# Kernel tuning notes

Measured on AMD Instinct MI355X. Metric: run time of the kernel, lower is better.

The kernel has to match this reference:

```python
import jax, jax.numpy as jnp
import numpy as np
from jax import lax

H = 128      # hidden width everywhere
L = 4        # GRU layers
N = 32768    # number of atom events / decode steps
V = 3072     # 512 * 6 atom vocab


def _lin(x, w, b):
    return x @ w.T + b


def _lrelu(x):
    return jnp.where(x >= 0, x, 0.2 * x)


def _res(x, w1, b1, w2, b2):
    h = _lrelu(_lin(x, w1, b1))
    return _lrelu(x + _lin(h, w2, b2))


def _res_stack(x, ws1, bs1, ws2, bs2):
    for i in range(ws1.shape[0]):
        x = _res(x, ws1[i], bs1[i], ws2[i], bs2[i])
    return x


def _head(x, ws1, bs1, ws2, bs2, w, b):
    return _lin(_res_stack(x, ws1, bs1, ws2, bs2), w, b)


def _forward(atom, time, mag, atom_emb, mag_w, mag_b, pos_w, pos_b,
             reduce_w, reduce_b, net_w1, net_b1, net_w2, net_b2,
             final_w, final_b, redg_w, redg_b, wg_w1, wg_b1, wg_w2, wg_b2,
             gfinal_w, gfinal_b, gru_wih, gru_whh, gru_bih, gru_bhh,
             ah_w1, ah_b1, ah_w2, ah_b2, ah_w, ah_b,
             ph_w1, ph_b1, ph_w2, ph_b2, ph_w, ph_b,
             mh_w1, mh_b1, mh_w2, mh_b2, mh_w, mh_b):
    n_steps = atom.shape[0]
    # ----- Encoder -----
    ae = atom_emb[atom]                               # [N, 128]
    te = _lin(time[:, None], pos_w, pos_b)            # [N, 128]
    me = _lin(mag[:, None], mag_w, mag_b)             # [N, 128]
    x = _lin(jnp.concatenate([ae, te, me], axis=-1), reduce_w, reduce_b)
    x = _res_stack(x, net_w1, net_b1, net_w2, net_b2)
    x = _lin(x, final_w, final_b)
    g = jnp.sum(x, axis=0, keepdims=True)             # [1, 128]
    x = jnp.concatenate([x, jnp.broadcast_to(g, x.shape)], axis=-1)
    x = _lin(x, redg_w, redg_b)
    x = _res_stack(x, wg_w1, wg_b1, wg_w2, wg_b2)
    x = _lin(x, gfinal_w, gfinal_b)
    z = jnp.sum(x, axis=0, keepdims=True)             # [1, 128]

    # ----- Decoder: 4-layer GRU, output fed back as next input -----
    def gru_step(carry, _):
        inp, hid = carry                              # [128], [L, 128]
        xs = inp
        new_h = []
        for l in range(L):
            gi = gru_wih[l] @ xs + gru_bih[l]         # [384]
            gh = gru_whh[l] @ hid[l] + gru_bhh[l]     # [384]
            ir, iz, inn = jnp.split(gi, 3)
            hr, hz, hn = jnp.split(gh, 3)
            r = jax.nn.sigmoid(ir + hr)
            zt = jax.nn.sigmoid(iz + hz)
            n = jnp.tanh(inn + r * hn)
            hl = (1.0 - zt) * n + zt * hid[l]
            new_h.append(hl)
            xs = hl
        return (xs, jnp.stack(new_h)), xs

    init = (z[0], jnp.zeros((L, H), dtype=z.dtype))
    _, encodings = lax.scan(gru_step, init, None, length=n_steps)  # [N, 128]

    atoms = _head(encodings, ah_w1, ah_b1, ah_w2, ah_b2, ah_w, ah_b)
    pos = jnp.clip(_head(encodings, ph_w1, ph_b1, ph_w2, ph_b2, ph_w, ph_b), 0.0, 1.0)
    mags = _head(encodings, mh_w1, mh_b1, mh_w2, mh_b2, mh_w, mh_b)
    return atoms, pos, mags, z


def setup_inputs():
    key = jax.random.key(0)
    ks = jax.random.split(key, 64)
    it = iter(range(64))

    def nrm(shape, scale=0.05):
        return jax.random.normal(ks[next(it)], shape, dtype=jnp.float32) * scale

    inp = {
        "atom": jax.random.randint(ks[next(it)], (N,), 0, V),
        "time": jax.random.uniform(ks[next(it)], (N,), dtype=jnp.float32),
        "mag": jax.random.uniform(ks[next(it)], (N,), dtype=jnp.float32),
        "atom_emb": nrm((V, H)),
        "mag_w": nrm((H, 1)), "mag_b": nrm((H,)),
        "pos_w": nrm((H, 1)), "pos_b": nrm((H,)),
        "reduce_w": nrm((H, 3 * H)), "reduce_b": nrm((H,)),
        "net_w1": nrm((4, H, H)), "net_b1": nrm((4, H)),
        "net_w2": nrm((4, H, H)), "net_b2": nrm((4, H)),
        "final_w": nrm((H, H)), "final_b": nrm((H,)),
        "redg_w": nrm((H, 2 * H)), "redg_b": nrm((H,)),
        "wg_w1": nrm((4, H, H)), "wg_b1": nrm((4, H)),
        "wg_w2": nrm((4, H, H)), "wg_b2": nrm((4, H)),
        "gfinal_w": nrm((H, H)), "gfinal_b": nrm((H,)),
        "gru_wih": nrm((L, 3 * H, H)), "gru_whh": nrm((L, 3 * H, H)),
        "gru_bih": nrm((L, 3 * H)), "gru_bhh": nrm((L, 3 * H)),
        "ah_w1": nrm((2, H, H)), "ah_b1": nrm((2, H)),
        "ah_w2": nrm((2, H, H)), "ah_b2": nrm((2, H)),
        "ah_w": nrm((H, H)), "ah_b": nrm((H,)),
        "ph_w1": nrm((2, H, H)), "ph_b1": nrm((2, H)),
        "ph_w2": nrm((2, H, H)), "ph_b2": nrm((2, H)),
        "ph_w": nrm((1, H)), "ph_b": nrm((1,)),
        "mh_w1": nrm((2, H, H)), "mh_b1": nrm((2, H)),
        "mh_w2": nrm((2, H, H)), "mh_b2": nrm((2, H)),
        "mh_w": nrm((1, H)), "mh_b": nrm((1,)),
    }
    return inp


def reference(atom, time, mag, atom_emb, mag_w, mag_b, pos_w, pos_b,
              reduce_w, reduce_b, net_w1, net_b1, net_w2, net_b2,
              final_w, final_b, redg_w, redg_b, wg_w1, wg_b1, wg_w2, wg_b2,
              gfinal_w, gfinal_b, gru_wih, gru_whh, gru_bih, gru_bhh,
              ah_w1, ah_b1, ah_w2, ah_b2, ah_w, ah_b,
              ph_w1, ph_b1, ph_w2, ph_b2, ph_w, ph_b,
              mh_w1, mh_b1, mh_w2, mh_b2, mh_w, mh_b):
    return _forward(atom, time, mag, atom_emb, mag_w, mag_b, pos_w, pos_b,
                    reduce_w, reduce_b, net_w1, net_b1, net_w2, net_b2,
                    final_w, final_b, redg_w, redg_b, wg_w1, wg_b1, wg_w2, wg_b2,
                    gfinal_w, gfinal_b, gru_wih, gru_whh, gru_bih, gru_bhh,
                    ah_w1, ah_b1, ah_w2, ah_b2, ah_w, ah_b,
                    ph_w1, ph_b1, ph_w2, ph_b2, ph_w, ph_b,
                    mh_w1, mh_b1, mh_w2, mh_b2, mh_w, mh_b)
```

## Files before the change

kernel.cpp:

```cpp
#include <hip/hip_runtime.h>
#include <hip/hip_bf16.h>

#define NEVT 32768
#define NBLK (NEVT / 8)

typedef _Float16 f16;
typedef _Float16 f16x2 __attribute__((ext_vector_type(2)));
typedef float f32x16 __attribute__((ext_vector_type(16)));
typedef float Row128[128];

#ifndef __has_builtin
#define __has_builtin(x) 0
#endif

__device__ __forceinline__ float dot2f(f16x2 a, f16x2 b, float c) {
#if __has_builtin(__builtin_amdgcn_fdot2)
  return __builtin_amdgcn_fdot2(a, b, c, false);
#else
  return c + (float)a[0] * (float)b[0] + (float)a[1] * (float)b[1];
#endif
}

__device__ __forceinline__ float lrelu(float v) { return v >= 0.f ? v : 0.2f * v; }

__device__ __forceinline__ float sigmoidf(float x) {
  return 1.f / (1.f + __expf(-x));
}

__device__ __forceinline__ float tanh_f(float x) {
  float ax = fabsf(x);
  float e = __expf(-2.f * ax);
  float t = (1.f - e) / (1.f + e);
  return x >= 0.f ? t : -t;
}

__device__ __forceinline__ void res_block(Row128* xb, Row128* hb,
    const float* __restrict__ w1, const float* __restrict__ b1,
    const float* __restrict__ w2, const float* __restrict__ b2, int u) {
  float acc[8];
  float bb = b1[u];
  #pragma unroll
  for (int r = 0; r < 8; ++r) acc[r] = bb;
  #pragma unroll 4
  for (int k = 0; k < 128; ++k) {
    float w = w1[u * 128 + k];
    #pragma unroll
    for (int r = 0; r < 8; ++r) acc[r] += w * xb[r][k];
  }
  #pragma unroll
  for (int r = 0; r < 8; ++r) hb[r][u] = lrelu(acc[r]);
  __syncthreads();
  bb = b2[u];
  #pragma unroll
  for (int r = 0; r < 8; ++r) acc[r] = bb;
  #pragma unroll 4
  for (int k = 0; k < 128; ++k) {
    float w = w2[u * 128 + k];
    #pragma unroll
    for (int r = 0; r < 8; ++r) acc[r] += w * hb[r][k];
  }
  #pragma unroll
  for (int r = 0; r < 8; ++r) xb[r][u] = lrelu(xb[r][u] + acc[r]);
  __syncthreads();
}

__global__ __launch_bounds__(128) void enc1_kernel(
    const int* __restrict__ atom, const float* __restrict__ tvec,
    const float* __restrict__ mvec, const float* __restrict__ atom_emb,
    const float* __restrict__ mag_w, const float* __restrict__ mag_b,
    const float* __restrict__ pos_w, const float* __restrict__ pos_b,
    const float* __restrict__ reduce_w, const float* __restrict__ reduce_b,
    const float* __restrict__ net_w1, const float* __restrict__ net_b1,
    const float* __restrict__ net_w2, const float* __restrict__ net_b2,
    const float* __restrict__ final_w, const float* __restrict__ final_b,
    float* __restrict__ xf, float* __restrict__ pg) {
  const int u = threadIdx.x;
  const int r0 = blockIdx.x * 8;
  __shared__ float xin[8][384];
  __shared__ float xb[8][128];
  __shared__ float hb[8][128];
  #pragma unroll
  for (int r = 0; r < 8; ++r) {
    int row = r0 + r;
    xin[r][u] = atom_emb[atom[row] * 128 + u];
    xin[r][128 + u] = tvec[row] * pos_w[u] + pos_b[u];
    xin[r][256 + u] = mvec[row] * mag_w[u] + mag_b[u];
  }
  __syncthreads();
  float acc[8];
  float bb = reduce_b[u];
  #pragma unroll
  for (int r = 0; r < 8; ++r) acc[r] = bb;
  #pragma unroll 4
  for (int k = 0; k < 384; ++k) {
    float w = reduce_w[u * 384 + k];
    #pragma unroll
    for (int r = 0; r < 8; ++r) acc[r] += w * xin[r][k];
  }
  #pragma unroll
  for (int r = 0; r < 8; ++r) xb[r][u] = acc[r];
  __syncthreads();
  for (int blk = 0; blk < 4; ++blk)
    res_block(xb, hb, net_w1 + blk * 16384, net_b1 + blk * 128,
              net_w2 + blk * 16384, net_b2 + blk * 128, u);
  bb = final_b[u];
  #pragma unroll
  for (int r = 0; r < 8; ++r) acc[r] = bb;
  #pragma unroll 4
  for (int k = 0; k < 128; ++k) {
    float w = final_w[u * 128 + k];
    #pragma unroll
    for (int r = 0; r < 8; ++r) acc[r] += w * xb[r][k];
  }
  float s = 0.f;
  #pragma unroll
  for (int r = 0; r < 8; ++r) {
    xf[(r0 + r) * 128 + u] = acc[r];
    s += acc[r];
  }
  pg[blockIdx.x * 128 + u] = s;
}

__global__ __launch_bounds__(1024) void reduce_kernel(
    const float* __restrict__ src, int m, float* __restrict__ dst) {
  int u = threadIdx.x & 127, c = threadIdx.x >> 7;
  float s = 0.f;
  for (int i = c; i < m; i += 8) s += src[i * 128 + u];
  __shared__ float tmp[8][128];
  tmp[c][u] = s;
  __syncthreads();
  if (c == 0) {
    float t = 0.f;
    #pragma unroll
    for (int j = 0; j < 8; ++j) t += tmp[j][u];
    dst[u] = t;
  }
}

__global__ __launch_bounds__(128) void enc2_kernel(
    const float* __restrict__ xf, const float* __restrict__ g,
    const float* __restrict__ redg_w, const float* __restrict__ redg_b,
    const float* __restrict__ wg_w1, const float* __restrict__ wg_b1,
    const float* __restrict__ wg_w2, const float* __restrict__ wg_b2,
    const float* __restrict__ gfinal_w, const float* __restrict__ gfinal_b,
    float* __restrict__ pz) {
  const int u = threadIdx.x;
  const int r0 = blockIdx.x * 8;
  __shared__ float xin[8][256];
  __shared__ float xb[8][128];
  __shared__ float hb[8][128];
  #pragma unroll
  for (int r = 0; r < 8; ++r) {
    xin[r][u] = xf[(r0 + r) * 128 + u];
    xin[r][128 + u] = g[u];
  }
  __syncthreads();
  float acc[8];
  float bb = redg_b[u];
  #pragma unroll
  for (int r = 0; r < 8; ++r) acc[r] = bb;
  #pragma unroll 4
  for (int k = 0; k < 256; ++k) {
    float w = redg_w[u * 256 + k];
    #pragma unroll
    for (int r = 0; r < 8; ++r) acc[r] += w * xin[r][k];
  }
  #pragma unroll
  for (int r = 0; r < 8; ++r) xb[r][u] = acc[r];
  __syncthreads();
  for (int blk = 0; blk < 4; ++blk)
    res_block(xb, hb, wg_w1 + blk * 16384, wg_b1 + blk * 128,
              wg_w2 + blk * 16384, wg_b2 + blk * 128, u);
  bb = gfinal_b[u];
  #pragma unroll
  for (int r = 0; r < 8; ++r) acc[r] = bb;
  #pragma unroll 4
  for (int k = 0; k < 128; ++k) {
    float w = gfinal_w[u * 128 + k];
    #pragma unroll
    for (int r = 0; r < 8; ++r) acc[r] += w * xb[r][k];
  }
  float s = 0.f;
  #pragma unroll
  for (int r = 0; r < 8; ++r) s += acc[r];
  pz[blockIdx.x * 128 + u] = s;
}

__global__ __launch_bounds__(256) void wprep_kernel(
    const float* __restrict__ wih, const float* __restrict__ whh,
    f16* __restrict__ w16i, f16* __restrict__ w16h) {
  int idx = blockIdx.x * 256 + threadIdx.x;
  if (idx < 196608) {
    w16i[idx] = (f16)wih[idx];
    w16h[idx] = (f16)whh[idx];
  }
}


#define PW(WV, K) __builtin_bit_cast(f16x2, (WV)[(K)])

#define D4(WV, B, Q, A) \
  A = dot2f(PW(WV,(B)+0), __builtin_bit_cast(f16x2,(Q).x), A); \
  A = dot2f(PW(WV,(B)+1), __builtin_bit_cast(f16x2,(Q).y), A); \
  A = dot2f(PW(WV,(B)+2), __builtin_bit_cast(f16x2,(Q).z), A); \
  A = dot2f(PW(WV,(B)+3), __builtin_bit_cast(f16x2,(Q).w), A);

#define D4Q(WQ, Q, A) \
  A = dot2f(__builtin_bit_cast(f16x2,(WQ).x), __builtin_bit_cast(f16x2,(Q).x), A); \
  A = dot2f(__builtin_bit_cast(f16x2,(WQ).y), __builtin_bit_cast(f16x2,(Q).y), A); \
  A = dot2f(__builtin_bit_cast(f16x2,(WQ).z), __builtin_bit_cast(f16x2,(Q).z), A); \
  A = dot2f(__builtin_bit_cast(f16x2,(WQ).w), __builtin_bit_cast(f16x2,(Q).w), A);

#define F32T(WV, K, XS, OFF) { f16x2 p_ = PW(WV, (K)); \
  a0_ += (float)p_[0] * (XS)[(OFF) + 2*(K)]; \
  a1_ += (float)p_[1] * (XS)[(OFF) + 2*(K) + 1]; }

#define F32T16(WV, XS, OFF) \
  F32T(WV,0,XS,OFF) F32T(WV,1,XS,OFF) F32T(WV,2,XS,OFF) F32T(WV,3,XS,OFF) \
  F32T(WV,4,XS,OFF) F32T(WV,5,XS,OFF) F32T(WV,6,XS,OFF) F32T(WV,7,XS,OFF) \
  F32T(WV,8,XS,OFF) F32T(WV,9,XS,OFF) F32T(WV,10,XS,OFF) F32T(WV,11,XS,OFF) \
  F32T(WV,12,XS,OFF) F32T(WV,13,XS,OFF) F32T(WV,14,XS,OFF) F32T(WV,15,XS,OFF)

#define L4(WV, I, Q) \
  (WV)[4*(I)+0] = (Q).x; (WV)[4*(I)+1] = (Q).y; \
  (WV)[4*(I)+2] = (Q).z; (WV)[4*(I)+3] = (Q).w;

#define LOAD_W16(WA, WB, BASE) do { \
  const float4* p_ = (const float4*)(BASE); \
  float4 q0_ = p_[0], q1_ = p_[1], q2_ = p_[2], q3_ = p_[3]; \
  float4 q4_ = p_[4], q5_ = p_[5], q6_ = p_[6], q7_ = p_[7]; \
  L4(WA, 0, q0_) L4(WA, 1, q1_) L4(WA, 2, q2_) L4(WA, 3, q3_) \
  L4(WB, 0, q4_) L4(WB, 1, q5_) L4(WB, 2, q6_) L4(WB, 3, q7_) \
} while (0)

#define PH_HEAD(L) \
  const float4* s4_ = (const float4*)(srcf + soff_base + (L) * sideOff); \
  const float4* wc4_ = (const float4*)(w16 + (wCb + (L) * 49152)); \
  float aA0_=0.f,aA1_=0.f,aB0_=0.f,aB1_=0.f,aC0_=0.f,aC1_=0.f; \
  float4 q0_, q1_, wq0_, wq1_;

#define PH_TAIL() \
  pgf[d0] = aA0_ + aA1_; pgf[d0+2] = aB0_ + aB1_; pgf[d0+4] = aC0_ + aC1_;

#define PH_R(L, Aa, Ab, Ba, Bb) do { PH_HEAD(L) \
  q0_=s4_[0]; q1_=s4_[1]; wq0_=wc4_[0]; wq1_=wc4_[1]; \
  D4(Aa,0,q0_,aA0_) D4(Aa,4,q1_,aA1_) D4(Ba,0,q0_,aB0_) D4(Ba,4,q1_,aB1_) \
  D4Q(wq0_,q0_,aC0_) D4Q(wq1_,q1_,aC1_) \
  q0_=s4_[2]; q1_=s4_[3]; wq0_=wc4_[2]; wq1_=wc4_[3]; \
  D4(Aa,8,q0_,aA0_) D4(Aa,12,q1_,aA1_) D4(Ba,8,q0_,aB0_) D4(Ba,12,q1_,aB1_) \
  D4Q(wq0_,q0_,aC0_) D4Q(wq1_,q1_,aC1_) \
  q0_=s4_[4]; q1_=s4_[5]; wq0_=wc4_[4]; wq1_=wc4_[5]; \
  D4(Ab,0,q0_,aA0_) D4(Ab,4,q1_,aA1_) D4(Bb,0,q0_,aB0_) D4(Bb,4,q1_,aB1_) \
  D4Q(wq0_,q0_,aC0_) D4Q(wq1_,q1_,aC1_) \
  q0_=s4_[6]; q1_=s4_[7]; wq0_=wc4_[6]; wq1_=wc4_[7]; \
  D4(Ab,8,q0_,aA0_) D4(Ab,12,q1_,aA1_) D4(Bb,8,q0_,aB0_) D4(Bb,12,q1_,aB1_) \
  D4Q(wq0_,q0_,aC0_) D4Q(wq1_,q1_,aC1_) \
  PH_TAIL() } while (0)

#define PH_L(L, Aa, Ab, WL) do { PH_HEAD(L) \
  float4 bw0_, bw1_; \
  q0_=s4_[0]; q1_=s4_[1]; wq0_=wc4_[0]; wq1_=wc4_[1]; \
  bw0_=(WL)[0*512+tid]; bw1_=(WL)[1*512+tid]; \
  D4(Aa,0,q0_,aA0_) D4(Aa,4,q1_,aA1_) D4Q(bw0_,q0_,aB0_) D4Q(bw1_,q1_,aB1_) \
  D4Q(wq0_,q0_,aC0_) D4Q(wq1_,q1_,aC1_) \
  q0_=s4_[2]; q1_=s4_[3]; wq0_=wc4_[2]; wq1_=wc4_[3]; \
  bw0_=(WL)[2*512+tid]; bw1_=(WL)[3*512+tid]; \
  D4(Aa,8,q0_,aA0_) D4(Aa,12,q1_,aA1_) D4Q(bw0_,q0_,aB0_) D4Q(bw1_,q1_,aB1_) \
  D4Q(wq0_,q0_,aC0_) D4Q(wq1_,q1_,aC1_) \
  q0_=s4_[4]; q1_=s4_[5]; wq0_=wc4_[4]; wq1_=wc4_[5]; \
  bw0_=(WL)[4*512+tid]; bw1_=(WL)[5*512+tid]; \
  D4(Ab,0,q0_,aA0_) D4(Ab,4,q1_,aA1_) D4Q(bw0_,q0_,aB0_) D4Q(bw1_,q1_,aB1_) \
  D4Q(wq0_,q0_,aC0_) D4Q(wq1_,q1_,aC1_) \
  q0_=s4_[6]; q1_=s4_[7]; wq0_=wc4_[6]; wq1_=wc4_[7]; \
  bw0_=(WL)[6*512+tid]; bw1_=(WL)[7*512+tid]; \
  D4(Ab,8,q0_,aA0_) D4(Ab,12,q1_,aA1_) D4Q(bw0_,q0_,aB0_) D4Q(bw1_,q1_,aB1_) \
  D4Q(wq0_,q0_,aC0_) D4Q(wq1_,q1_,aC1_) \
  PH_TAIL() } while (0)

#define GATE(L, T) \
  if (tid < 128) { \
    const float2* gi2_ = (const float2*)pgf; \
    const float2* gh2_ = (const float2*)(pgf + 768); \
    float2 ar_ = gi2_[tid],      br_ = gh2_[tid]; \
    float2 az_ = gi2_[128+tid],  bz_ = gh2_[128+tid]; \
    float2 an_ = gi2_[256+tid],  bn_ = gh2_[256+tid]; \
    float r_ = sigmoidf((ar_.x + ar_.y) + (br_.x + br_.y) + bsum_r[L][tid]); \
    float z_ = sigmoidf((az_.x + az_.y) + (bz_.x + bz_.y) + bsum_z[L][tid]); \
    float n_ = tanh_f((an_.x + an_.y) + b_in[L][tid] + \
                      r_ * ((bn_.x + bn_.y) + b_hn[L][tid])); \
    float h_ = (1.f - z_) * n_ + z_ * h32[L][tid]; \
    h32[L][tid] = h_; f16 hh_ = (f16)h_; \
    srcbuf[(1 + (L)) * 128 + tid] = hh_; srcbuf[tid] = hh_; \
    if ((L) == 3) enc[(size_t)(T) * 128 + tid] = h_; \
  }

__global__ __attribute__((amdgpu_flat_work_group_size(512, 512)))
__attribute__((amdgpu_waves_per_eu(2, 2))) void gru_kernel(
    const f16* __restrict__ w16, const float* __restrict__ bih,
    const float* __restrict__ bhh, const float* __restrict__ zvec,
    float* __restrict__ enc) {
  const int tid = threadIdx.x;

  __shared__ __align__(16) float4 wldsB2[4096];
  __shared__ __align__(16) float4 wldsB3[4096];
  __shared__ __align__(16) float pgbuf[1536];
  __shared__ __align__(16) f16 srcbuf[640];
  __shared__ __align__(16) float h32[4][128];
  __shared__ __align__(16) float cur32[128];
  __shared__ float bsum_r[4][128], bsum_z[4][128];
  __shared__ float b_in[4][128], b_hn[4][128];

  float* const pgf = pgbuf;
  const f16* const srcf = srcbuf;

  const int side = tid >> 8;
  const int ti = tid & 255;
  const int half = ti & 1;
  const int hs = half * 64;
  const int rb = 3 * (ti >> 1);
  const int d0 = side * 768 + rb * 2 + half;
  const int soff_base = side ? (128 + hs) : hs;
  const int sideOff = side * 128;
  const int wAb_ = side * 196608 + rb * 128 + hs;
  const int wCb = wAb_ + 256;

  f32x16 rA0a, rA0b, rA1a, rA1b, rA2a, rA2b, rA3a, rA3b, rB0a, rB0b, rB1a, rB1b;
  LOAD_W16(rA0a, rA0b, w16 + wAb_);
  LOAD_W16(rA1a, rA1b, w16 + wAb_ + 49152);
  LOAD_W16(rA2a, rA2b, w16 + wAb_ + 2 * 49152);
  LOAD_W16(rA3a, rA3b, w16 + wAb_ + 3 * 49152);
  LOAD_W16(rB0a, rB0b, w16 + wAb_ + 128);
  LOAD_W16(rB1a, rB1b, w16 + wAb_ + 49152 + 128);
  asm volatile("" : "+v"(rA0a), "+v"(rA0b), "+v"(rA1a), "+v"(rA1b),
                    "+v"(rA2a), "+v"(rA2b));
  asm volatile("" : "+v"(rA3a), "+v"(rA3b), "+v"(rB0a), "+v"(rB0b),
                    "+v"(rB1a), "+v"(rB1b));

  {
    const float4* p2 = (const float4*)(w16 + wAb_ + 2 * 49152 + 128);
    const float4* p3 = (const float4*)(w16 + wAb_ + 3 * 49152 + 128);
    #pragma unroll
    for (int c = 0; c < 8; ++c) {
      wldsB2[c * 512 + tid] = p2[c];
      wldsB3[c * 512 + tid] = p3[c];
    }
  }

  if (tid < 128) {
    cur32[tid] = zvec[tid];
    srcbuf[tid] = (f16)0.f;
    #pragma unroll
    for (int l = 0; l < 4; ++l) {
      h32[l][tid] = 0.f;
      srcbuf[(1 + l) * 128 + tid] = (f16)0.f;
    }
  }
  {
    int l_ = tid >> 7, row_ = tid & 127;
    bsum_r[l_][row_] = bih[l_*384 + row_]       + bhh[l_*384 + row_];
    bsum_z[l_][row_] = bih[l_*384 + 128 + row_] + bhh[l_*384 + 128 + row_];
    b_in[l_][row_]   = bih[l_*384 + 256 + row_];
    b_hn[l_][row_]   = bhh[l_*384 + 256 + row_];
  }
  __syncthreads();

  {
    if (tid < 256) {
      const float* xs_ = cur32 + hs;
      { float a0_ = 0.f, a1_ = 0.f;
        F32T16(rA0a, xs_, 0) F32T16(rA0b, xs_, 32)
        pgf[d0] = a0_ + a1_; }
      { float a0_ = 0.f, a1_ = 0.f;
        F32T16(rB0a, xs_, 0) F32T16(rB0b, xs_, 32)
        pgf[d0 + 2] = a0_ + a1_; }
      { float a0_ = 0.f, a1_ = 0.f;
        const f16x2* wp_ = (const f16x2*)(w16 + wCb);
        for (int k = 0; k < 32; ++k) {
          f16x2 w_ = wp_[k];
          a0_ += (float)w_[0] * xs_[2 * k];
          a1_ += (float)w_[1] * xs_[2 * k + 1];
        }
        pgf[d0 + 4] = a0_ + a1_; }
    } else {
      PH_R(0, rA0a, rA0b, rB0a, rB0b);
    }
    __syncthreads();
    GATE(0, 0)
    __syncthreads();
    PH_R(1, rA1a, rA1b, rB1a, rB1b);
    __syncthreads();
    GATE(1, 0)
    __syncthreads();
    PH_L(2, rA2a, rA2b, wldsB2);
    __syncthreads();
    GATE(2, 0)
    __syncthreads();
    PH_L(3, rA3a, rA3b, wldsB3);
    __syncthreads();
    GATE(3, 0)
    __syncthreads();
  }

  #pragma unroll 1
  for (int t = 1; t < NEVT; ++t) {
    PH_R(0, rA0a, rA0b, rB0a, rB0b);
    __syncthreads();
    GATE(0, t)
    __syncthreads();
    PH_R(1, rA1a, rA1b, rB1a, rB1b);
    __syncthreads();
    GATE(1, t)
    __syncthreads();
    PH_L(2, rA2a, rA2b, wldsB2);
    __syncthreads();
    GATE(2, t)
    __syncthreads();
    PH_L(3, rA3a, rA3b, wldsB3);
    __syncthreads();
    GATE(3, t)
    __syncthreads();
  }
}

__global__ __launch_bounds__(128) void heads_kernel(
    const float* __restrict__ enc,
    const float* __restrict__ ah_w1, const float* __restrict__ ah_b1,
    const float* __restrict__ ah_w2, const float* __restrict__ ah_b2,
    const float* __restrict__ ah_w, const float* __restrict__ ah_b,
    const float* __restrict__ ph_w1, const float* __restrict__ ph_b1,
    const float* __restrict__ ph_w2, const float* __restrict__ ph_b2,
    const float* __restrict__ ph_w, const float* __restrict__ ph_b,
    const float* __restrict__ mh_w1, const float* __restrict__ mh_b1,
    const float* __restrict__ mh_w2, const float* __restrict__ mh_b2,
    const float* __restrict__ mh_w, const float* __restrict__ mh_b,
    float* __restrict__ oa, float* __restrict__ op, float* __restrict__ om) {
  const int u = threadIdx.x;
  const int r0 = blockIdx.x * 8;
  __shared__ float eb[8][128], xb[8][128], hb[8][128];
  #pragma unroll
  for (int r = 0; r < 8; ++r) eb[r][u] = enc[(size_t)(r0 + r) * 128 + u];
  #pragma unroll
  for (int r = 0; r < 8; ++r) xb[r][u] = eb[r][u];
  __syncthreads();
  for (int blk = 0; blk < 2; ++blk)
    res_block(xb, hb, ah_w1 + blk * 16384, ah_b1 + blk * 128,
              ah_w2 + blk * 16384, ah_b2 + blk * 128, u);
  {
    float acc[8];
    float bb = ah_b[u];
    #pragma unroll
    for (int r = 0; r < 8; ++r) acc[r] = bb;
    #pragma unroll 4
    for (int k = 0; k < 128; ++k) {
      float w = ah_w[u * 128 + k];
      #pragma unroll
      for (int r = 0; r < 8; ++r) acc[r] += w * xb[r][k];
    }
    #pragma unroll
    for (int r = 0; r < 8; ++r) oa[(size_t)(r0 + r) * 128 + u] = acc[r];
  }
  __syncthreads();
  #pragma unroll
  for (int r = 0; r < 8; ++r) xb[r][u] = eb[r][u];
  __syncthreads();
  for (int blk = 0; blk < 2; ++blk)
    res_block(xb, hb, ph_w1 + blk * 16384, ph_b1 + blk * 128,
              ph_w2 + blk * 16384, ph_b2 + blk * 128, u);
  if (u < 8) {
    int r = u;
    float s = ph_b[0];
    for (int k = 0; k < 128; ++k) s += ph_w[k] * xb[r][k];
    s = s < 0.f ? 0.f : (s > 1.f ? 1.f : s);
    op[r0 + r] = s;
  }
  __syncthreads();
  #pragma unroll
  for (int r = 0; r < 8; ++r) xb[r][u] = eb[r][u];
  __syncthreads();
  for (int blk = 0; blk < 2; ++blk)
    res_block(xb, hb, mh_w1 + blk * 16384, mh_b1 + blk * 128,
              mh_w2 + blk * 16384, mh_b2 + blk * 128, u);
  if (u < 8) {
    int r = u;
    float s = mh_b[0];
    for (int k = 0; k < 128; ++k) s += mh_w[k] * xb[r][k];
    om[r0 + r] = s;
  }
}

extern "C" void kernel_launch(void* const* d_in, const int* in_sizes, int n_in,
                              void* d_out, int out_size, void* d_ws, size_t ws_size,
                              hipStream_t stream) {
  const int* atom = (const int*)d_in[0];
  const float* tvec = (const float*)d_in[1];
  const float* mvec = (const float*)d_in[2];
  const float* atom_emb = (const float*)d_in[3];
  const float* mag_w = (const float*)d_in[4];
  const float* mag_b = (const float*)d_in[5];
  const float* pos_w = (const float*)d_in[6];
  const float* pos_b = (const float*)d_in[7];
  const float* reduce_w = (const float*)d_in[8];
  const float* reduce_b = (const float*)d_in[9];
  const float* net_w1 = (const float*)d_in[10];
  const float* net_b1 = (const float*)d_in[11];
  const float* net_w2 = (const float*)d_in[12];
  const float* net_b2 = (const float*)d_in[13];
  const float* final_w = (const float*)d_in[14];
  const float* final_b = (const float*)d_in[15];
  const float* redg_w = (const float*)d_in[16];
  const float* redg_b = (const float*)d_in[17];
  const float* wg_w1 = (const float*)d_in[18];
  const float* wg_b1 = (const float*)d_in[19];
  const float* wg_w2 = (const float*)d_in[20];
  const float* wg_b2 = (const float*)d_in[21];
  const float* gfinal_w = (const float*)d_in[22];
  const float* gfinal_b = (const float*)d_in[23];
  const float* gru_wih = (const float*)d_in[24];
  const float* gru_whh = (const float*)d_in[25];
  const float* gru_bih = (const float*)d_in[26];
  const float* gru_bhh = (const float*)d_in[27];
  const float* ah_w1 = (const float*)d_in[28];
  const float* ah_b1 = (const float*)d_in[29];
  const float* ah_w2 = (const float*)d_in[30];
  const float* ah_b2 = (const float*)d_in[31];
  const float* ah_w = (const float*)d_in[32];
  const float* ah_b = (const float*)d_in[33];
  const float* ph_w1 = (const float*)d_in[34];
  const float* ph_b1 = (const float*)d_in[35];
  const float* ph_w2 = (const float*)d_in[36];
  const float* ph_b2 = (const float*)d_in[37];
  const float* ph_w = (const float*)d_in[38];
  const float* ph_b = (const float*)d_in[39];
  const float* mh_w1 = (const float*)d_in[40];
  const float* mh_b1 = (const float*)d_in[41];
  const float* mh_w2 = (const float*)d_in[42];
  const float* mh_b2 = (const float*)d_in[43];
  const float* mh_w = (const float*)d_in[44];
  const float* mh_b = (const float*)d_in[45];

  float* out = (float*)d_out;
  float* oa = out;
  float* op = out + (size_t)NEVT * 128;
  float* om = op + NEVT;
  float* oz = om + NEVT;

  float* enc = (float*)d_ws;
  float* pg = enc + (size_t)NEVT * 128;
  float* pz = pg + (size_t)NBLK * 128;
  float* gv = pz + (size_t)NBLK * 128;
  float* xf = oa;

  f16* w16i = (f16*)pg;
  f16* w16h = w16i + 196608;

  enc1_kernel<<<NBLK, 128, 0, stream>>>(atom, tvec, mvec, atom_emb, mag_w, mag_b,
      pos_w, pos_b, reduce_w, reduce_b, net_w1, net_b1, net_w2, net_b2,
      final_w, final_b, xf, pg);
  reduce_kernel<<<1, 1024, 0, stream>>>(pg, NBLK, gv);
  wprep_kernel<<<768, 256, 0, stream>>>(gru_wih, gru_whh, w16i, w16h);
  enc2_kernel<<<NBLK, 128, 0, stream>>>(xf, gv, redg_w, redg_b, wg_w1, wg_b1,
      wg_w2, wg_b2, gfinal_w, gfinal_b, pz);
  reduce_kernel<<<1, 1024, 0, stream>>>(pz, NBLK, oz);
  gru_kernel<<<1, 512, 0, stream>>>(w16i, gru_bih, gru_bhh, oz, enc);
  heads_kernel<<<NBLK, 128, 0, stream>>>(enc, ah_w1, ah_b1, ah_w2, ah_b2, ah_w, ah_b,
      ph_w1, ph_b1, ph_w2, ph_b2, ph_w, ph_b, mh_w1, mh_b1, mh_w2, mh_b2, mh_w, mh_b,
      oa, op, om);
}
```

Before: 108.6 ms.

## Store GRU weights as scaled FP8 and decode on the fly in the recurrence

Quantizes GRU input and hidden weights to FP8 (E4M3, scaled by 256) in the prep kernel. The sequential GRU kernel then reads these compact weights from global/L2 each step and converts them to f16 pairs before the dot2 products. This replaces the large f16 register-resident weight arrays and the per-step global f16 loads of the third gate. The aim is to cut weight traffic and register pressure on the serial critical path, at the cost of extra conversion instructions per step, reduced accuracy, and a dead manual decoder left in the code.

```diff
diff --git a/kernel.cpp b/kernel.cpp
--- a/kernel.cpp
+++ b/kernel.cpp
@@ -6,8 +6,8 @@
 
 typedef _Float16 f16;
 typedef _Float16 f16x2 __attribute__((ext_vector_type(2)));
-typedef float f32x16 __attribute__((ext_vector_type(16)));
 typedef float Row128[128];
+typedef unsigned int uint32;
 
 #ifndef __has_builtin
 #define __has_builtin(x) 0
@@ -18,6 +18,45 @@
   return __builtin_amdgcn_fdot2(a, b, c, false);
 #else
   return c + (float)a[0] * (float)b[0] + (float)a[1] * (float)b[1];
+#endif
+}
+
+__device__ __forceinline__ f16x2 dec2_manual(uint32 two) {
+  uint32 b0 = two & 0xff, b1 = (two >> 8) & 0xff;
+  uint32 em0 = b0 & 0x7f, em1 = b1 & 0x7f;
+  uint32 h0 = ((b0 & 0x80) << 8) | ((em0 < 8) ? 0u : ((em0 << 7) + 0x2000));
+  uint32 h1 = ((b1 & 0x80) << 8) | ((em1 < 8) ? 0u : ((em1 << 7) + 0x2000));
+  return __builtin_bit_cast(f16x2, (unsigned short)(h0) | (h1 << 16) |
+                                   (h0 & 0xffff) ? (h0 | (h1 << 16)) : (h1 << 16));
+}
+__device__ __forceinline__ f16x2 dec2(uint32 two) {
+#if __has_builtin(__builtin_amdgcn_cvt_pk_f16_fp8)
+  return __builtin_amdgcn_cvt_pk_f16_fp8((short)two);
+#else
+  uint32 b0 = two & 0xff, b1 = (two >> 8) & 0xff;
+  uint32 em0 = b0 & 0x7f, em1 = b1 & 0x7f;
+  uint32 h0 = ((b0 & 0x80) << 8) | ((em0 < 8) ? 0u : ((em0 << 7) + 0x2000));
+  uint32 h1 = ((b1 & 0x80) << 8) | ((em1 < 8) ? 0u : ((em1 << 7) + 0x2000));
+  return __builtin_bit_cast(f16x2, h0 | (h1 << 16));
+#endif
+}
+__device__ __forceinline__ f16x2 cvt8lo(uint32 d) { return dec2(d & 0xffff); }
+__device__ __forceinline__ f16x2 cvt8hi(uint32 d) { return dec2(d >> 16); }
+
+__device__ __forceinline__ uint32 enc_fp8(float f) {
+#if __has_builtin(__builtin_amdgcn_cvt_pk_fp8_f32)
+  return (uint32)__builtin_amdgcn_cvt_pk_fp8_f32(f, f, 0, false) & 0xff;
+#else
+  uint32 u = __builtin_bit_cast(uint32, f);
+  uint32 s = (u >> 24) & 0x80;
+  int E = (int)((u >> 23) & 0xff) - 127 + 7;
+  uint32 m = u & 0x7fffff;
+  if (E <= 0) return s;
+  uint32 keep = m >> 20, rest = m & 0xfffff;
+  uint32 rnd = keep + ((rest > 0x80000u) || (rest == 0x80000u && (keep & 1)));
+  if (rnd == 8) { rnd = 0; E += 1; }
+  if (E >= 16) return s | 0x7e;
+  return s | ((uint32)E << 3) | rnd;
 #endif
 }
 
@@ -186,96 +225,95 @@
   pz[blockIdx.x * 128 + u] = s;
 }
 
+#define FP8_SCALE 256.0f
 __global__ __launch_bounds__(256) void wprep_kernel(
     const float* __restrict__ wih, const float* __restrict__ whh,
-    f16* __restrict__ w16i, f16* __restrict__ w16h) {
+    f16* __restrict__ w16i, f16* __restrict__ w16h,
+    unsigned char* __restrict__ w8) {
   int idx = blockIdx.x * 256 + threadIdx.x;
   if (idx < 196608) {
     w16i[idx] = (f16)wih[idx];
     w16h[idx] = (f16)whh[idx];
   }
-}
-
-
-#define PW(WV, K) __builtin_bit_cast(f16x2, (WV)[(K)])
-
-#define D4(WV, B, Q, A) \
-  A = dot2f(PW(WV,(B)+0), __builtin_bit_cast(f16x2,(Q).x), A); \
-  A = dot2f(PW(WV,(B)+1), __builtin_bit_cast(f16x2,(Q).y), A); \
-  A = dot2f(PW(WV,(B)+2), __builtin_bit_cast(f16x2,(Q).z), A); \
-  A = dot2f(PW(WV,(B)+3), __builtin_bit_cast(f16x2,(Q).w), A);
-
-#define D4Q(WQ, Q, A) \
-  A = dot2f(__builtin_bit_cast(f16x2,(WQ).x), __builtin_bit_cast(f16x2,(Q).x), A); \
-  A = dot2f(__builtin_bit_cast(f16x2,(WQ).y), __builtin_bit_cast(f16x2,(Q).y), A); \
-  A = dot2f(__builtin_bit_cast(f16x2,(WQ).z), __builtin_bit_cast(f16x2,(Q).z), A); \
-  A = dot2f(__builtin_bit_cast(f16x2,(WQ).w), __builtin_bit_cast(f16x2,(Q).w), A);
-
-#define F32T(WV, K, XS, OFF) { f16x2 p_ = PW(WV, (K)); \
-  a0_ += (float)p_[0] * (XS)[(OFF) + 2*(K)]; \
-  a1_ += (float)p_[1] * (XS)[(OFF) + 2*(K) + 1]; }
-
-#define F32T16(WV, XS, OFF) \
-  F32T(WV,0,XS,OFF) F32T(WV,1,XS,OFF) F32T(WV,2,XS,OFF) F32T(WV,3,XS,OFF) \
-  F32T(WV,4,XS,OFF) F32T(WV,5,XS,OFF) F32T(WV,6,XS,OFF) F32T(WV,7,XS,OFF) \
-  F32T(WV,8,XS,OFF) F32T(WV,9,XS,OFF) F32T(WV,10,XS,OFF) F32T(WV,11,XS,OFF) \
-  F32T(WV,12,XS,OFF) F32T(WV,13,XS,OFF) F32T(WV,14,XS,OFF) F32T(WV,15,XS,OFF)
-
-#define L4(WV, I, Q) \
-  (WV)[4*(I)+0] = (Q).x; (WV)[4*(I)+1] = (Q).y; \
-  (WV)[4*(I)+2] = (Q).z; (WV)[4*(I)+3] = (Q).w;
-
-#define LOAD_W16(WA, WB, BASE) do { \
-  const float4* p_ = (const float4*)(BASE); \
-  float4 q0_ = p_[0], q1_ = p_[1], q2_ = p_[2], q3_ = p_[3]; \
-  float4 q4_ = p_[4], q5_ = p_[5], q6_ = p_[6], q7_ = p_[7]; \
-  L4(WA, 0, q0_) L4(WA, 1, q1_) L4(WA, 2, q2_) L4(WA, 3, q3_) \
-  L4(WB, 0, q4_) L4(WB, 1, q5_) L4(WB, 2, q6_) L4(WB, 3, q7_) \
-} while (0)
+  if (idx < 49152) {
+    uint32 di = 0, dh = 0;
+    #pragma unroll
+    for (int j = 0; j < 4; ++j) {
+      di |= enc_fp8(wih[4 * idx + j] * FP8_SCALE) << (8 * j);
+      dh |= enc_fp8(whh[4 * idx + j] * FP8_SCALE) << (8 * j);
+    }
+    ((uint32*)w8)[idx] = di;
+    ((uint32*)w8)[49152 + idx] = dh;
+  }
+}
+
+
+#define SCI (1.f / FP8_SCALE)
+
+#define D16(U, Qa, Qb, A0, A1) \
+  A0 = dot2f(cvt8lo((U).x), __builtin_bit_cast(f16x2, (Qa).x), A0); \
+  A1 = dot2f(cvt8hi((U).x), __builtin_bit_cast(f16x2, (Qa).y), A1); \
+  A0 = dot2f(cvt8lo((U).y), __builtin_bit_cast(f16x2, (Qa).z), A0); \
+  A1 = dot2f(cvt8hi((U).y), __builtin_bit_cast(f16x2, (Qa).w), A1); \
+  A0 = dot2f(cvt8lo((U).z), __builtin_bit_cast(f16x2, (Qb).x), A0); \
+  A1 = dot2f(cvt8hi((U).z), __builtin_bit_cast(f16x2, (Qb).y), A1); \
+  A0 = dot2f(cvt8lo((U).w), __builtin_bit_cast(f16x2, (Qb).z), A0); \
+  A1 = dot2f(cvt8hi((U).w), __builtin_bit_cast(f16x2, (Qb).w), A1);
+
+#define D8L(W, Q, A0, A1) \
+  A0 = dot2f(__builtin_bit_cast(f16x2,(W).x), __builtin_bit_cast(f16x2,(Q).x), A0); \
+  A1 = dot2f(__builtin_bit_cast(f16x2,(W).y), __builtin_bit_cast(f16x2,(Q).y), A1); \
+  A0 = dot2f(__builtin_bit_cast(f16x2,(W).z), __builtin_bit_cast(f16x2,(Q).z), A0); \
+  A1 = dot2f(__builtin_bit_cast(f16x2,(W).w), __builtin_bit_cast(f16x2,(Q).w), A1);
 
 #define PH_HEAD(L) \
   const float4* s4_ = (const float4*)(srcf + soff_base + (L) * sideOff); \
-  const float4* wc4_ = (const float4*)(w16 + (wCb + (L) * 49152)); \
-  float aA0_=0.f,aA1_=0.f,aB0_=0.f,aB1_=0.f,aC0_=0.f,aC1_=0.f; \
-  float4 q0_, q1_, wq0_, wq1_;
-
-#define PH_TAIL() \
-  pgf[d0] = aA0_ + aA1_; pgf[d0+2] = aB0_ + aB1_; pgf[d0+4] = aC0_ + aC1_;
-
-#define PH_R(L, Aa, Ab, Ba, Bb) do { PH_HEAD(L) \
-  q0_=s4_[0]; q1_=s4_[1]; wq0_=wc4_[0]; wq1_=wc4_[1]; \
-  D4(Aa,0,q0_,aA0_) D4(Aa,4,q1_,aA1_) D4(Ba,0,q0_,aB0_) D4(Ba,4,q1_,aB1_) \
-  D4Q(wq0_,q0_,aC0_) D4Q(wq1_,q1_,aC1_) \
-  q0_=s4_[2]; q1_=s4_[3]; wq0_=wc4_[2]; wq1_=wc4_[3]; \
-  D4(Aa,8,q0_,aA0_) D4(Aa,12,q1_,aA1_) D4(Ba,8,q0_,aB0_) D4(Ba,12,q1_,aB1_) \
-  D4Q(wq0_,q0_,aC0_) D4Q(wq1_,q1_,aC1_) \
-  q0_=s4_[4]; q1_=s4_[5]; wq0_=wc4_[4]; wq1_=wc4_[5]; \
-  D4(Ab,0,q0_,aA0_) D4(Ab,4,q1_,aA1_) D4(Bb,0,q0_,aB0_) D4(Bb,4,q1_,aB1_) \
-  D4Q(wq0_,q0_,aC0_) D4Q(wq1_,q1_,aC1_) \
-  q0_=s4_[6]; q1_=s4_[7]; wq0_=wc4_[6]; wq1_=wc4_[7]; \
-  D4(Ab,8,q0_,aA0_) D4(Ab,12,q1_,aA1_) D4(Bb,8,q0_,aB0_) D4(Bb,12,q1_,aB1_) \
-  D4Q(wq0_,q0_,aC0_) D4Q(wq1_,q1_,aC1_) \
-  PH_TAIL() } while (0)
-
-#define PH_L(L, Aa, Ab, WL) do { PH_HEAD(L) \
-  float4 bw0_, bw1_; \
-  q0_=s4_[0]; q1_=s4_[1]; wq0_=wc4_[0]; wq1_=wc4_[1]; \
-  bw0_=(WL)[0*512+tid]; bw1_=(WL)[1*512+tid]; \
-  D4(Aa,0,q0_,aA0_) D4(Aa,4,q1_,aA1_) D4Q(bw0_,q0_,aB0_) D4Q(bw1_,q1_,aB1_) \
-  D4Q(wq0_,q0_,aC0_) D4Q(wq1_,q1_,aC1_) \
-  q0_=s4_[2]; q1_=s4_[3]; wq0_=wc4_[2]; wq1_=wc4_[3]; \
-  bw0_=(WL)[2*512+tid]; bw1_=(WL)[3*512+tid]; \
-  D4(Aa,8,q0_,aA0_) D4(Aa,12,q1_,aA1_) D4Q(bw0_,q0_,aB0_) D4Q(bw1_,q1_,aB1_) \
-  D4Q(wq0_,q0_,aC0_) D4Q(wq1_,q1_,aC1_) \
-  q0_=s4_[4]; q1_=s4_[5]; wq0_=wc4_[4]; wq1_=wc4_[5]; \
-  bw0_=(WL)[4*512+tid]; bw1_=(WL)[5*512+tid]; \
-  D4(Ab,0,q0_,aA0_) D4(Ab,4,q1_,aA1_) D4Q(bw0_,q0_,aB0_) D4Q(bw1_,q1_,aB1_) \
-  D4Q(wq0_,q0_,aC0_) D4Q(wq1_,q1_,aC1_) \
-  q0_=s4_[6]; q1_=s4_[7]; wq0_=wc4_[6]; wq1_=wc4_[7]; \
-  bw0_=(WL)[6*512+tid]; bw1_=(WL)[7*512+tid]; \
-  D4(Ab,8,q0_,aA0_) D4(Ab,12,q1_,aA1_) D4Q(bw0_,q0_,aB0_) D4Q(bw1_,q1_,aB1_) \
-  D4Q(wq0_,q0_,aC0_) D4Q(wq1_,q1_,aC1_) \
-  PH_TAIL() } while (0)
+  float4 q0_=s4_[0],q1_=s4_[1],q2_=s4_[2],q3_=s4_[3]; \
+  float4 q4_=s4_[4],q5_=s4_[5],q6_=s4_[6],q7_=s4_[7]; \
+  float aA0_=0.f,aA1_=0.f,aB0_=0.f,aB1_=0.f,aC0_=0.f,aC1_=0.f;
+
+#define PH_S(L) do { \
+  const uint4* wa_ = (const uint4*)(w8 + wAb_ + (L) * 49152); \
+  const uint4* wb_ = (const uint4*)(w8 + wAb_ + (L) * 49152 + 128); \
+  const uint4* wc_ = (const uint4*)(w8 + wAb_ + (L) * 49152 + 256); \
+  uint4 ua0=wa_[0],ua1=wa_[1],ua2=wa_[2],ua3=wa_[3]; \
+  uint4 ub0=wb_[0],ub1=wb_[1],ub2=wb_[2],ub3=wb_[3]; \
+  uint4 uc0=wc_[0],uc1=wc_[1],uc2=wc_[2],uc3=wc_[3]; \
+  PH_HEAD(L) \
+  D16(ua0,q0_,q1_,aA0_,aA1_) D16(ua1,q2_,q3_,aA0_,aA1_) \
+  D16(ua2,q4_,q5_,aA0_,aA1_) D16(ua3,q6_,q7_,aA0_,aA1_) \
+  D16(ub0,q0_,q1_,aB0_,aB1_) D16(ub1,q2_,q3_,aB0_,aB1_) \
+  D16(ub2,q4_,q5_,aB0_,aB1_) D16(ub3,q6_,q7_,aB0_,aB1_) \
+  D16(uc0,q0_,q1_,aC0_,aC1_) D16(uc1,q2_,q3_,aC0_,aC1_) \
+  D16(uc2,q4_,q5_,aC0_,aC1_) D16(uc3,q6_,q7_,aC0_,aC1_) \
+  pgf[d0]     = (aA0_ + aA1_) * SCI; \
+  pgf[d0 + 2] = (aB0_ + aB1_) * SCI; \
+  pgf[d0 + 4] = (aC0_ + aC1_) * SCI; \
+} while (0)
+
+#define PH_LB(L, WL) do { \
+  const uint4* wa_ = (const uint4*)(w8 + wAb_ + (L) * 49152); \
+  const uint4* wc_ = (const uint4*)(w8 + wAb_ + (L) * 49152 + 256); \
+  uint4 ua0=wa_[0],ua1=wa_[1],ua2=wa_[2],ua3=wa_[3]; \
+  uint4 uc0=wc_[0],uc1=wc_[1],uc2=wc_[2],uc3=wc_[3]; \
+  PH_HEAD(L) \
+  D16(ua0,q0_,q1_,aA0_,aA1_) D16(ua1,q2_,q3_,aA0_,aA1_) \
+  D16(ua2,q4_,q5_,aA0_,aA1_) D16(ua3,q6_,q7_,aA0_,aA1_) \
+  { float4 w_; \
+    w_=(WL)[0*512+tid]; D8L(w_,q0_,aB0_,aB1_) \
+    w_=(WL)[1*512+tid]; D8L(w_,q1_,aB0_,aB1_) \
+    w_=(WL)[2*512+tid]; D8L(w_,q2_,aB0_,aB1_) \
+    w_=(WL)[3*512+tid]; D8L(w_,q3_,aB0_,aB1_) \
+    w_=(WL)[4*512+tid]; D8L(w_,q4_,aB0_,aB1_) \
+    w_=(WL)[5*512+tid]; D8L(w_,q5_,aB0_,aB1_) \
+    w_=(WL)[6*512+tid]; D8L(w_,q6_,aB0_,aB1_) \
+    w_=(WL)[7*512+tid]; D8L(w_,q7_,aB0_,aB1_) } \
+  D16(uc0,q0_,q1_,aC0_,aC1_) D16(uc1,q2_,q3_,aC0_,aC1_) \
+  D16(uc2,q4_,q5_,aC0_,aC1_) D16(uc3,q6_,q7_,aC0_,aC1_) \
+  pgf[d0]     = (aA0_ + aA1_) * SCI; \
+  pgf[d0 + 2] = (aB0_ + aB1_); \
+  pgf[d0 + 4] = (aC0_ + aC1_) * SCI; \
+} while (0)
 
 #define GATE(L, T) \
   if (tid < 128) { \
@@ -296,9 +334,9 @@
 
 __global__ __attribute__((amdgpu_flat_work_group_size(512, 512)))
 __attribute__((amdgpu_waves_per_eu(2, 2))) void gru_kernel(
-    const f16* __restrict__ w16, const float* __restrict__ bih,
-    const float* __restrict__ bhh, const float* __restrict__ zvec,
-    float* __restrict__ enc) {
+    const f16* __restrict__ w16, const unsigned char* __restrict__ w8,
+    const float* __restrict__ bih, const float* __restrict__ bhh,
+    const float* __restrict__ zvec, float* __restrict__ enc) {
   const int tid = threadIdx.x;
 
   __shared__ __align__(16) float4 wldsB2[4096];
@@ -322,19 +360,6 @@
   const int soff_base = side ? (128 + hs) : hs;
   const int sideOff = side * 128;
   const int wAb_ = side * 196608 + rb * 128 + hs;
-  const int wCb = wAb_ + 256;
-
-  f32x16 rA0a, rA0b, rA1a, rA1b, rA2a, rA2b, rA3a, rA3b, rB0a, rB0b, rB1a, rB1b;
-  LOAD_W16(rA0a, rA0b, w16 + wAb_);
-  LOAD_W16(rA1a, rA1b, w16 + wAb_ + 49152);
-  LOAD_W16(rA2a, rA2b, w16 + wAb_ + 2 * 49152);
-  LOAD_W16(rA3a, rA3b, w16 + wAb_ + 3 * 49152);
-  LOAD_W16(rB0a, rB0b, w16 + wAb_ + 128);
-  LOAD_W16(rB1a, rB1b, w16 + wAb_ + 49152 + 128);
-  asm volatile("" : "+v"(rA0a), "+v"(rA0b), "+v"(rA1a), "+v"(rA1b),
-                    "+v"(rA2a), "+v"(rA2b));
-  asm volatile("" : "+v"(rA3a), "+v"(rA3b), "+v"(rB0a), "+v"(rB0b),
-                    "+v"(rB1a), "+v"(rB1b));
 
   {
     const float4* p2 = (const float4*)(w16 + wAb_ + 2 * 49152 + 128);
@@ -367,35 +392,34 @@
   {
     if (tid < 256) {
       const float* xs_ = cur32 + hs;
-      { float a0_ = 0.f, a1_ = 0.f;
-        F32T16(rA0a, xs_, 0) F32T16(rA0b, xs_, 32)
-        pgf[d0] = a0_ + a1_; }
-      { float a0_ = 0.f, a1_ = 0.f;
-        F32T16(rB0a, xs_, 0) F32T16(rB0b, xs_, 32)
-        pgf[d0 + 2] = a0_ + a1_; }
-      { float a0_ = 0.f, a1_ = 0.f;
-        const f16x2* wp_ = (const f16x2*)(w16 + wCb);
-        for (int k = 0; k < 32; ++k) {
-          f16x2 w_ = wp_[k];
-          a0_ += (float)w_[0] * xs_[2 * k];
-          a1_ += (float)w_[1] * xs_[2 * k + 1];
+      #pragma unroll
+      for (int rr = 0; rr < 3; ++rr) {
+        const uint32* wp_ = (const uint32*)(w8 + wAb_ + rr * 128);
+        float a0_ = 0.f, a1_ = 0.f;
+        #pragma unroll
+        for (int k = 0; k < 16; ++k) {
+          uint32 d_ = wp_[k];
+          f16x2 lo_ = cvt8lo(d_), hi_ = cvt8hi(d_);
+          a0_ += (float)lo_[0] * xs_[4*k]     + (float)hi_[0] * xs_[4*k + 2];
+          a1_ += (float)lo_[1] * xs_[4*k + 1] + (float)hi_[1] * xs_[4*k + 3];
         }
-        pgf[d0 + 4] = a0_ + a1_; }
+        pgf[d0 + 2 * rr] = (a0_ + a1_) * SCI;
+      }
     } else {
-      PH_R(0, rA0a, rA0b, rB0a, rB0b);
+      PH_S(0);
     }
     __syncthreads();
     GATE(0, 0)
     __syncthreads();
-    PH_R(1, rA1a, rA1b, rB1a, rB1b);
+    PH_S(1);
     __syncthreads();
     GATE(1, 0)
     __syncthreads();
-    PH_L(2, rA2a, rA2b, wldsB2);
+    PH_LB(2, wldsB2);
     __syncthreads();
     GATE(2, 0)
     __syncthreads();
-    PH_L(3, rA3a, rA3b, wldsB3);
+    PH_LB(3, wldsB3);
     __syncthreads();
     GATE(3, 0)
     __syncthreads();
@@ -403,19 +427,19 @@
 
   #pragma unroll 1
   for (int t = 1; t < NEVT; ++t) {
-    PH_R(0, rA0a, rA0b, rB0a, rB0b);
+    PH_S(0);
     __syncthreads();
     GATE(0, t)
     __syncthreads();
-    PH_R(1, rA1a, rA1b, rB1a, rB1b);
+    PH_S(1);
     __syncthreads();
     GATE(1, t)
     __syncthreads();
-    PH_L(2, rA2a, rA2b, wldsB2);
+    PH_LB(2, wldsB2);
     __syncthreads();
     GATE(2, t)
     __syncthreads();
-    PH_L(3, rA3a, rA3b, wldsB3);
+    PH_LB(3, wldsB3);
     __syncthreads();
     GATE(3, t)
     __syncthreads();
@@ -552,16 +576,17 @@
 
   f16* w16i = (f16*)pg;
   f16* w16h = w16i + 196608;
+  unsigned char* w8 = (unsigned char*)(w16i + 2 * 196608);
 
   enc1_kernel<<<NBLK, 128, 0, stream>>>(atom, tvec, mvec, atom_emb, mag_w, mag_b,
       pos_w, pos_b, reduce_w, reduce_b, net_w1, net_b1, net_w2, net_b2,
       final_w, final_b, xf, pg);
   reduce_kernel<<<1, 1024, 0, stream>>>(pg, NBLK, gv);
-  wprep_kernel<<<768, 256, 0, stream>>>(gru_wih, gru_whh, w16i, w16h);
+  wprep_kernel<<<768, 256, 0, stream>>>(gru_wih, gru_whh, w16i, w16h, w8);
   enc2_kernel<<<NBLK, 128, 0, stream>>>(xf, gv, redg_w, redg_b, wg_w1, wg_b1,
       wg_w2, wg_b2, gfinal_w, gfinal_b, pz);
   reduce_kernel<<<1, 1024, 0, stream>>>(pz, NBLK, oz);
-  gru_kernel<<<1, 512, 0, stream>>>(w16i, gru_bih, gru_bhh, oz, enc);
+  gru_kernel<<<1, 512, 0, stream>>>(w16i, w8, gru_bih, gru_bhh, oz, enc);
   heads_kernel<<<NBLK, 128, 0, stream>>>(enc, ah_w1, ah_b1, ah_w2, ah_b2, ah_w, ah_b,
       ph_w1, ph_b1, ph_w2, ph_b2, ph_w, ph_b, mh_w1, mh_b1, mh_w2, mh_b2, mh_w, mh_b,
       oa, op, om);
```

Result: slower. 424.4 ms (+290.7%).
